# Kernel optimization log

Hardware: AMD Instinct MI355X
Metric: run time of the kernel (lower is better)

Reference implementation:

```python
import jax, jax.numpy as jnp
import numpy as np

B, S, A, H, NH = 4, 4096, 512, 1024, 16
HD = H // NH  # 64


def setup_inputs() -> dict:
    key = jax.random.key(0)
    ks = jax.random.split(key, 12)
    s = 1.0 / np.sqrt(H)
    return {
        "hidden_states": jax.random.normal(ks[0], (B, S, H), jnp.float32),
        "audio_tokens": jax.random.normal(ks[1], (B, A, H), jnp.float32),
        "attention_mask": jax.random.randint(ks[2], (B, A), 0, 2, jnp.int32),
        "Wq": jax.random.normal(ks[3], (H, H), jnp.float32) * s,
        "bq": jnp.zeros((H,), jnp.float32),
        "Wk": jax.random.normal(ks[4], (H, H), jnp.float32) * s,
        "bk": jnp.zeros((H,), jnp.float32),
        "Wv": jax.random.normal(ks[5], (H, H), jnp.float32) * s,
        "bv": jnp.zeros((H,), jnp.float32),
        "Wo": jax.random.normal(ks[6], (H, H), jnp.float32) * s,
        "bo": jnp.zeros((H,), jnp.float32),
        "ln_gamma": jnp.ones((H,), jnp.float32),
        "ln_beta": jnp.zeros((H,), jnp.float32),
        "residual_scale": jnp.asarray(0.05, jnp.float32),
    }


def _san(x, big=10000.0):
    return jnp.nan_to_num(x, nan=0.0, posinf=big, neginf=-big)


def reference(hidden_states, audio_tokens, attention_mask, Wq, bq, Wk, bk, Wv, bv,
              Wo, bo, ln_gamma, ln_beta, residual_scale):
    hs = _san(hidden_states).astype(jnp.float32)
    at = _san(audio_tokens).astype(jnp.float32)

    def heads(x, W, b):  # [b, t, H] -> [b, t, nh, hd]
        return _san(x @ W.T + b).reshape(x.shape[0], x.shape[1], NH, HD)

    q = heads(hs, Wq, bq)            # [B,S,NH,HD]
    k = heads(at, Wk, bk)            # [B,A,NH,HD]
    v = heads(at, Wv, bv)            # [B,A,NH,HD]

    scale = max(np.sqrt(HD), 1e-8)
    scores = jnp.einsum("bsnd,band->bnsa", q, k) / scale  # [B,NH,S,A]
    scores = jnp.clip(_san(jnp.clip(scores, -50.0, 50.0), 50.0), -50.0, 50.0)

    attend = (attention_mask > 0)[:, None, None, :]       # [B,1,1,A]
    scores = jnp.where(attend, scores, -10000.0)
    scores = jnp.clip(scores, -50.0, 50.0)

    probs = jax.nn.softmax(scores, axis=-1)
    probs = _san(probs, 1.0)
    probs = probs / (jnp.sum(probs, axis=-1, keepdims=True) + 1e-8)

    ctx = jnp.einsum("bnsa,band->bsnd", probs, v).reshape(B, S, H)
    delta = _san(ctx @ Wo.T + bo)

    rs = jnp.clip(residual_scale, 0.0, 0.3)
    delta = rs * delta

    mu = jnp.mean(delta, axis=-1, keepdims=True)
    var = jnp.mean(jnp.square(delta - mu), axis=-1, keepdims=True)
    delta = (delta - mu) / jnp.sqrt(var + 1e-5) * ln_gamma + ln_beta
    return delta
```

## Files before the change

### kernel.cpp

```cpp
#include <hip/hip_runtime.h>
#include <hip/hip_bf16.h>
#include <cstdint>
#include <cstddef>

#define B_  4
#define S_  4096
#define A_  512
#define H_  1024
#define NH_ 16
#define HD_ 64

typedef __bf16 bf16;
typedef __bf16 bf16x8 __attribute__((ext_vector_type(8)));
typedef __bf16 bf16x4 __attribute__((ext_vector_type(4)));
typedef float  fx4    __attribute__((ext_vector_type(4)));

typedef __attribute__((address_space(3))) void LDS_v;
typedef const __attribute__((address_space(1))) void GLB_v;

#define CSTRIDE 136

__device__ __forceinline__ void gl_lds16(const void* g, void* l) {
    __builtin_amdgcn_global_load_lds((GLB_v*)g, (LDS_v*)l, 16, 0, 0);
}

__device__ __forceinline__ float sanf(float x) {
    if (x != x) return 0.f;
    if (fabsf(x) == __builtin_inff()) return x > 0.f ? 10000.f : -10000.f;
    return x;
}

__global__ __launch_bounds__(256) void cast_all(const float* __restrict__ hs,
                                                const float* __restrict__ at,
                                                const float* __restrict__ wq,
                                                const float* __restrict__ wk,
                                                const float* __restrict__ wv,
                                                const float* __restrict__ wo,
                                                bf16* __restrict__ dhs, bf16* __restrict__ dat,
                                                bf16* __restrict__ dwq, bf16* __restrict__ dwk,
                                                bf16* __restrict__ dwv, bf16* __restrict__ dwo) {
    int i = blockIdx.x * 256 + threadIdx.x;
    const float* s; bf16* d; int off;
    if (i < 4194304)      { s = hs; d = dhs; off = i; }
    else if (i < 4718592) { s = at; d = dat; off = i - 4194304; }
    else if (i < 4980736) { s = wq; d = dwq; off = i - 4718592; }
    else if (i < 5242880) { s = wk; d = dwk; off = i - 4980736; }
    else if (i < 5505024) { s = wv; d = dwv; off = i - 5242880; }
    else                  { s = wo; d = dwo; off = i - 5505024; }
    float4 v = ((const float4*)s)[off];
    bf16x4 o;
    o[0] = (bf16)sanf(v.x); o[1] = (bf16)sanf(v.y);
    o[2] = (bf16)sanf(v.z); o[3] = (bf16)sanf(v.w);
    *(bf16x4*)&d[(size_t)off * 4] = o;
}

__global__ __launch_bounds__(256) void qkv_gemm(const bf16* __restrict__ hsb,
                                                const bf16* __restrict__ atb,
                                                const bf16* __restrict__ wqb,
                                                const bf16* __restrict__ wkb,
                                                const bf16* __restrict__ wvb,
                                                const float* __restrict__ bq,
                                                const float* __restrict__ bk,
                                                const float* __restrict__ bv,
                                                bf16* __restrict__ Qb,
                                                bf16* __restrict__ Kb,
                                                bf16* __restrict__ Vtb) {
    __shared__ __align__(16) bf16 smem[128 * CSTRIDE];
    bf16* As = smem;
    bf16* Bs = smem + 128 * 32;
    bf16* Cs = smem;

    const int id = blockIdx.x;
    int mode, m0, n0;
    const bf16 *A, *Bt; const float* bias;
    if (id < 1024)      { mode = 0; m0 = (id & 127) * 128; n0 = (id >> 7) * 128; A = hsb; Bt = wqb; bias = bq; }
    else if (id < 1152) { int t = id - 1024; mode = 1; m0 = (t & 15) * 128; n0 = (t >> 4) * 128; A = atb; Bt = wkb; bias = bk; }
    else                { int t = id - 1152; mode = 2; m0 = (t & 15) * 128; n0 = (t >> 4) * 128; A = atb; Bt = wvb; bias = bv; }

    const int tid  = threadIdx.x;
    const int lane = tid & 63;
    const int wv   = tid >> 6;
    const int wr   = wv >> 1, wc = wv & 1;
    const int lr   = lane & 15, kq = lane >> 4;

    fx4 acc[4][4] = {};

    const bf16* Ag = A  + (size_t)m0 * 1024;
    const bf16* Bg = Bt + (size_t)n0 * 1024;
    const int c0 = tid, c1 = tid + 256;
    const int row0 = c0 >> 2, kc0 = c0 & 3;
    const int row1 = c1 >> 2, kc1 = c1 & 3;

    for (int k0 = 0; k0 < 1024; k0 += 32) {
        gl_lds16(Ag + (size_t)row0 * 1024 + k0 + kc0 * 8, &As[c0 * 8]);
        gl_lds16(Ag + (size_t)row1 * 1024 + k0 + kc1 * 8, &As[c1 * 8]);
        gl_lds16(Bg + (size_t)row0 * 1024 + k0 + kc0 * 8, &Bs[c0 * 8]);
        gl_lds16(Bg + (size_t)row1 * 1024 + k0 + kc1 * 8, &Bs[c1 * 8]);
        __syncthreads();
        bf16x8 af[4], bfr[4];
#pragma unroll
        for (int i = 0; i < 4; i++) af[i]  = *(const bf16x8*)&As[(wr * 64 + i * 16 + lr) * 32 + kq * 8];
#pragma unroll
        for (int j = 0; j < 4; j++) bfr[j] = *(const bf16x8*)&Bs[(wc * 64 + j * 16 + lr) * 32 + kq * 8];
#pragma unroll
        for (int i = 0; i < 4; i++)
#pragma unroll
            for (int j = 0; j < 4; j++)
                acc[i][j] = __builtin_amdgcn_mfma_f32_16x16x32_bf16(af[i], bfr[j], acc[i][j], 0, 0, 0);
        __syncthreads();
    }

    float bb[4];
#pragma unroll
    for (int j = 0; j < 4; j++) bb[j] = bias[n0 + wc * 64 + j * 16 + lr];

    if (mode == 2) {
#pragma unroll
        for (int i = 0; i < 4; i++) {
            int m = m0 + wr * 64 + i * 16 + kq * 4;
            int bidx = m >> 9, a = m & 511;
#pragma unroll
            for (int j = 0; j < 4; j++) {
                int col = n0 + wc * 64 + j * 16 + lr;
                bf16x4 o;
#pragma unroll
                for (int r = 0; r < 4; r++) o[r] = (bf16)(acc[i][j][r] + bb[j]);
                *(bf16x4*)&Vtb[((size_t)bidx * H_ + col) * A_ + a] = o;
            }
        }
    } else {
        const float sc = (mode == 0) ? 0.18033688011112042f : 1.0f;
#pragma unroll
        for (int i = 0; i < 4; i++) {
            int rowb = wr * 64 + i * 16 + kq * 4;
#pragma unroll
            for (int j = 0; j < 4; j++) {
                int col = wc * 64 + j * 16 + lr;
#pragma unroll
                for (int r = 0; r < 4; r++)
                    Cs[(rowb + r) * CSTRIDE + col] = (bf16)((acc[i][j][r] + bb[j]) * sc);
            }
        }
        __syncthreads();
        bf16* outp = (mode == 0) ? Qb : Kb;
#pragma unroll
        for (int p = 0; p < 8; p++) {
            int c = tid + p * 256, row = c >> 4, cc = (c & 15) * 8;
            *(bf16x8*)&outp[(size_t)(m0 + row) * 1024 + n0 + cc] = *(const bf16x8*)&Cs[row * CSTRIDE + cc];
        }
    }
}

__global__ __launch_bounds__(256) void gemm_o(const bf16* __restrict__ A,
                                              const bf16* __restrict__ Bt,
                                              const float* __restrict__ bias,
                                              bf16* __restrict__ C,
                                              const float* __restrict__ rsp) {
    __shared__ __align__(16) bf16 smem[128 * CSTRIDE];
    bf16* As = smem;
    bf16* Bs = smem + 128 * 32;
    bf16* Cs = smem;

    const int tid  = threadIdx.x;
    const int lane = tid & 63;
    const int wv   = tid >> 6;
    const int wr   = wv >> 1, wc = wv & 1;
    const int lr   = lane & 15, kq = lane >> 4;
    const int m0   = blockIdx.x * 128, n0 = blockIdx.y * 128;

    fx4 acc[4][4] = {};

    const bf16* Ag = A  + (size_t)m0 * 1024;
    const bf16* Bg = Bt + (size_t)n0 * 1024;
    const int c0 = tid, c1 = tid + 256;
    const int row0 = c0 >> 2, kc0 = c0 & 3;
    const int row1 = c1 >> 2, kc1 = c1 & 3;

    for (int k0 = 0; k0 < 1024; k0 += 32) {
        gl_lds16(Ag + (size_t)row0 * 1024 + k0 + kc0 * 8, &As[c0 * 8]);
        gl_lds16(Ag + (size_t)row1 * 1024 + k0 + kc1 * 8, &As[c1 * 8]);
        gl_lds16(Bg + (size_t)row0 * 1024 + k0 + kc0 * 8, &Bs[c0 * 8]);
        gl_lds16(Bg + (size_t)row1 * 1024 + k0 + kc1 * 8, &Bs[c1 * 8]);
        __syncthreads();
        bf16x8 af[4], bfr[4];
#pragma unroll
        for (int i = 0; i < 4; i++) af[i]  = *(const bf16x8*)&As[(wr * 64 + i * 16 + lr) * 32 + kq * 8];
#pragma unroll
        for (int j = 0; j < 4; j++) bfr[j] = *(const bf16x8*)&Bs[(wc * 64 + j * 16 + lr) * 32 + kq * 8];
#pragma unroll
        for (int i = 0; i < 4; i++)
#pragma unroll
            for (int j = 0; j < 4; j++)
                acc[i][j] = __builtin_amdgcn_mfma_f32_16x16x32_bf16(af[i], bfr[j], acc[i][j], 0, 0, 0);
        __syncthreads();
    }

    float bb[4];
#pragma unroll
    for (int j = 0; j < 4; j++) bb[j] = bias[n0 + wc * 64 + j * 16 + lr];
    float rs = fminf(fmaxf(rsp[0], 0.f), 0.3f);

#pragma unroll
    for (int i = 0; i < 4; i++) {
        int rowb = wr * 64 + i * 16 + kq * 4;
#pragma unroll
        for (int j = 0; j < 4; j++) {
            int col = wc * 64 + j * 16 + lr;
#pragma unroll
            for (int r = 0; r < 4; r++)
                Cs[(rowb + r) * CSTRIDE + col] = (bf16)(rs * (acc[i][j][r] + bb[j]));
        }
    }
    __syncthreads();
#pragma unroll
    for (int p = 0; p < 8; p++) {
        int c = tid + p * 256, row = c >> 4, cc = (c & 15) * 8;
        *(bf16x8*)&C[(size_t)(m0 + row) * 1024 + n0 + cc] = *(const bf16x8*)&Cs[row * CSTRIDE + cc];
    }
}

__global__ __launch_bounds__(256, 4) void attn_kernel(const bf16* __restrict__ Q,
                                                      const bf16* __restrict__ Kb,
                                                      const bf16* __restrict__ Vt,
                                                      const int* __restrict__ mask,
                                                      bf16* __restrict__ ctx) {
    __shared__ __align__(16) bf16 Qs[128 * 72];
    __shared__ __align__(16) bf16 Ks[64 * 72];
    __shared__ __align__(16) bf16 Vts[64 * 72];
    __shared__ float smask[512];
    __shared__ float dnm[128];

    const int tid  = threadIdx.x;
    const int lane = tid & 63;
    const int wv   = tid >> 6;
    const int lr   = lane & 15, kq = lane >> 4;
    const int st = blockIdx.x, h = blockIdx.y, b = blockIdx.z;
    const int m0 = b * S_ + st * 128;
    const float LO = -72.134752f;

    bf16x8 qtmp[4];
#pragma unroll
    for (int i = 0; i < 4; i++) {
        int c = tid + i * 256, row = c >> 3, ch = c & 7;
        qtmp[i] = *(const bf16x8*)(Q + (size_t)(m0 + row) * H_ + h * 64 + ch * 8);
    }
    smask[tid]       = (mask[b * A_ + tid] > 0)       ? -LO : LO;
    smask[tid + 256] = (mask[b * A_ + tid + 256] > 0) ? -LO : LO;
#pragma unroll
    for (int i = 0; i < 4; i++) {
        int c = tid + i * 256, row = c >> 3, ch = c & 7;
        *(bf16x8*)&Qs[row * 72 + ch * 8] = qtmp[i];
    }

    const int srow = tid >> 2, sseg = tid & 3;
    const size_t kg = (size_t)(b * A_ + srow) * H_ + h * 64 + sseg * 16;
    const bf16* vrow = Vt + (size_t)(b * H_ + h * 64 + srow) * A_;
    const int va0 = 32 * (sseg >> 1) + 4 * ((2 * sseg) & 3);
    const int va1 = 32 * (sseg >> 1) + 4 * ((2 * sseg + 1) & 3);

    bf16x8 kr0 = *(const bf16x8*)(Kb + kg);
    bf16x8 kr1 = *(const bf16x8*)(Kb + kg + 8);
    bf16x4 v00 = *(const bf16x4*)(vrow + va0);
    bf16x4 v01 = *(const bf16x4*)(vrow + va0 + 16);
    bf16x4 v10 = *(const bf16x4*)(vrow + va1);
    bf16x4 v11 = *(const bf16x4*)(vrow + va1 + 16);

    fx4 acco[2][4] = {};
    float dloc[2] = {0.f, 0.f};

    for (int it = 0; it < 8; it++) {
        const int a0 = it * 64;
        __syncthreads();
        *(bf16x8*)&Ks[srow * 72 + sseg * 16]      = kr0;
        *(bf16x8*)&Ks[srow * 72 + sseg * 16 + 8]  = kr1;
        *(bf16x8*)&Vts[srow * 72 + sseg * 16] =
            __builtin_shufflevector(v00, v01, 0, 1, 2, 3, 4, 5, 6, 7);
        *(bf16x8*)&Vts[srow * 72 + sseg * 16 + 8] =
            __builtin_shufflevector(v10, v11, 0, 1, 2, 3, 4, 5, 6, 7);
        __syncthreads();

        if (it < 7) {
            const size_t ko = kg + (size_t)(a0 + 64) * H_;
            kr0 = *(const bf16x8*)(Kb + ko);
            kr1 = *(const bf16x8*)(Kb + ko + 8);
            v00 = *(const bf16x4*)(vrow + a0 + 64 + va0);
            v01 = *(const bf16x4*)(vrow + a0 + 64 + va0 + 16);
            v10 = *(const bf16x4*)(vrow + a0 + 64 + va1);
            v11 = *(const bf16x4*)(vrow + a0 + 64 + va1 + 16);
        }

        fx4 accs[4][2] = {};
#pragma unroll
        for (int kk = 0; kk < 64; kk += 32) {
            bf16x8 kf[4], qf[2];
#pragma unroll
            for (int mt = 0; mt < 4; mt++)
                kf[mt] = *(const bf16x8*)&Ks[(mt * 16 + lr) * 72 + kk + kq * 8];
#pragma unroll
            for (int nt = 0; nt < 2; nt++)
                qf[nt] = *(const bf16x8*)&Qs[(wv * 32 + nt * 16 + lr) * 72 + kk + kq * 8];
#pragma unroll
            for (int mt = 0; mt < 4; mt++)
#pragma unroll
                for (int nt = 0; nt < 2; nt++)
                    accs[mt][nt] = __builtin_amdgcn_mfma_f32_16x16x32_bf16(kf[mt], qf[nt], accs[mt][nt], 0, 0, 0);
        }

        bf16x4 pf[4][2];
#pragma unroll
        for (int mt = 0; mt < 4; mt++) {
            fx4 cap = *(const fx4*)&smask[a0 + mt * 16 + kq * 4];
#pragma unroll
            for (int nt = 0; nt < 2; nt++) {
#pragma unroll
                for (int r = 0; r < 4; r++) {
                    float s2 = fmaxf(fminf(accs[mt][nt][r], cap[r]), LO);
                    float p  = __builtin_amdgcn_exp2f(s2);
                    pf[mt][nt][r] = (bf16)p;
                    dloc[nt] += p;
                }
            }
        }

#pragma unroll
        for (int ks = 0; ks < 2; ks++) {
            bf16x8 pa[2];
#pragma unroll
            for (int stl = 0; stl < 2; stl++)
                pa[stl] = __builtin_shufflevector(pf[2 * ks][stl], pf[2 * ks + 1][stl],
                                                  0, 1, 2, 3, 4, 5, 6, 7);
#pragma unroll
            for (int dt = 0; dt < 4; dt++) {
                bf16x8 vf = *(const bf16x8*)&Vts[(dt * 16 + lr) * 72 + ks * 32 + kq * 8];
#pragma unroll
                for (int stl = 0; stl < 2; stl++)
                    acco[stl][dt] = __builtin_amdgcn_mfma_f32_16x16x32_bf16(pa[stl], vf, acco[stl][dt], 0, 0, 0);
            }
        }
    }

#pragma unroll
    for (int nt = 0; nt < 2; nt++) {
        dloc[nt] += __shfl_xor(dloc[nt], 16);
        dloc[nt] += __shfl_xor(dloc[nt], 32);
    }
    if (kq == 0) {
        dnm[wv * 32 + lr]      = dloc[0];
        dnm[wv * 32 + 16 + lr] = dloc[1];
    }
    __syncthreads();

#pragma unroll
    for (int stl = 0; stl < 2; stl++) {
        fx4 dv = *(const fx4*)&dnm[wv * 32 + stl * 16 + kq * 4];
        float ri[4];
#pragma unroll
        for (int r = 0; r < 4; r++) ri[r] = __builtin_amdgcn_rcpf(dv[r]);
#pragma unroll
        for (int dt = 0; dt < 4; dt++)
#pragma unroll
            for (int r = 0; r < 4; r++)
                Qs[(wv * 32 + stl * 16 + kq * 4 + r) * 72 + dt * 16 + lr] =
                    (bf16)(acco[stl][dt][r] * ri[r]);
    }
    __syncthreads();
#pragma unroll
    for (int i = 0; i < 4; i++) {
        int c = tid + i * 256, row = c >> 3, ch = c & 7;
        *(bf16x8*)&ctx[(size_t)(m0 + row) * H_ + h * 64 + ch * 8] = *(const bf16x8*)&Qs[row * 72 + ch * 8];
    }
}

__global__ __launch_bounds__(256) void ln_kernel(const bf16* __restrict__ in,
                                                 float* __restrict__ out,
                                                 const float* __restrict__ gamma,
                                                 const float* __restrict__ beta) {
    __shared__ float red[8];
    const int tid = threadIdx.x;
    bf16x4 xb = *(const bf16x4*)&in[(size_t)blockIdx.x * 1024 + tid * 4];
    float x0 = (float)xb[0], x1 = (float)xb[1], x2 = (float)xb[2], x3 = (float)xb[3];
    float s = x0 + x1 + x2 + x3;
    float q = x0 * x0 + x1 * x1 + x2 * x2 + x3 * x3;
#pragma unroll
    for (int off = 32; off > 0; off >>= 1) {
        s += __shfl_down(s, off);
        q += __shfl_down(q, off);
    }
    if ((tid & 63) == 0) { red[(tid >> 6) * 2] = s; red[(tid >> 6) * 2 + 1] = q; }
    __syncthreads();
    s = red[0] + red[2] + red[4] + red[6];
    q = red[1] + red[3] + red[5] + red[7];
    float mean = s * (1.f / 1024.f);
    float var  = q * (1.f / 1024.f) - mean * mean;
    float inv  = rsqrtf(var + 1e-5f);
    float4 g  = ((const float4*)gamma)[tid];
    float4 bb = ((const float4*)beta)[tid];
    float4 y;
    y.x = (x0 - mean) * inv * g.x + bb.x;
    y.y = (x1 - mean) * inv * g.y + bb.y;
    y.z = (x2 - mean) * inv * g.z + bb.z;
    y.w = (x3 - mean) * inv * g.w + bb.w;
    ((float4*)(out + (size_t)blockIdx.x * 1024))[tid] = y;
}

extern "C" void kernel_launch(void* const* d_in, const int* in_sizes, int n_in,
                              void* d_out, int out_size, void* d_ws, size_t ws_size,
                              hipStream_t stream) {
    const float* hs    = (const float*)d_in[0];
    const float* at    = (const float*)d_in[1];
    const int*   maskp = (const int*)d_in[2];
    const float* Wq    = (const float*)d_in[3];
    const float* bq    = (const float*)d_in[4];
    const float* Wk    = (const float*)d_in[5];
    const float* bk    = (const float*)d_in[6];
    const float* Wv    = (const float*)d_in[7];
    const float* bv    = (const float*)d_in[8];
    const float* Wo    = (const float*)d_in[9];
    const float* bo    = (const float*)d_in[10];
    const float* gamma = (const float*)d_in[11];
    const float* beta  = (const float*)d_in[12];
    const float* rsp   = (const float*)d_in[13];

    char* ws = (char*)d_ws;
    bf16* hsb = (bf16*)(ws + 0);
    bf16* ctx = (bf16*)(ws + 0);
    bf16* atb = (bf16*)(ws + 33554432);
    bf16* wqb = (bf16*)(ws + 37748736);
    bf16* wkb = (bf16*)(ws + 39845888);
    bf16* wvb = (bf16*)(ws + 41943040);
    bf16* wob = (bf16*)(ws + 44040192);
    bf16* Qb  = (bf16*)(ws + 46137344);
    bf16* Ob  = Qb;
    bf16* Kb  = (bf16*)(ws + 79691776);
    bf16* Vtb = (bf16*)(ws + 83886080);

    cast_all<<<22528, 256, 0, stream>>>(hs, at, Wq, Wk, Wv, Wo,
                                        hsb, atb, wqb, wkb, wvb, wob);

    qkv_gemm<<<1280, 256, 0, stream>>>(hsb, atb, wqb, wkb, wvb,
                                       bq, bk, bv, Qb, Kb, Vtb);

    attn_kernel<<<dim3(32, 16, 4), 256, 0, stream>>>(Qb, Kb, Vtb, maskp, ctx);

    gemm_o<<<dim3(128, 8), 256, 0, stream>>>(ctx, wob, bo, Ob, rsp);
    ln_kernel<<<16384, 256, 0, stream>>>(Ob, (float*)d_out, gamma, beta);
}
```

Measured before the change: 327.8 us.

## Fuse fp32-to-bf16 casting into GEMM loads and drop separate cast kernel

Removes the standalone cast_all kernel and has qkv_gemm and gemm_o read fp32 inputs and weights directly, converting to bf16 in registers before storing to LDS. It uses register prefetch of the next k-tile in place of the async global_load_lds path, and writes epilogue outputs straight to global memory instead of staging them through LDS. This avoids a full write and re-read of bf16 copies of hidden states and weights, but doubles the global bytes each GEMM tile reads. Epilogue stores become narrow scattered bf16 writes. The NaN/inf sanitization of inputs is also dropped.

```diff
diff --git a/kernel.cpp b/kernel.cpp
--- a/kernel.cpp
+++ b/kernel.cpp
@@ -15,88 +15,77 @@
 typedef __bf16 bf16x4 __attribute__((ext_vector_type(4)));
 typedef float  fx4    __attribute__((ext_vector_type(4)));
 
-typedef __attribute__((address_space(3))) void LDS_v;
-typedef const __attribute__((address_space(1))) void GLB_v;
-
-#define CSTRIDE 136
-
-__device__ __forceinline__ void gl_lds16(const void* g, void* l) {
-    __builtin_amdgcn_global_load_lds((GLB_v*)g, (LDS_v*)l, 16, 0, 0);
-}
-
-__device__ __forceinline__ float sanf(float x) {
-    if (x != x) return 0.f;
-    if (fabsf(x) == __builtin_inff()) return x > 0.f ? 10000.f : -10000.f;
-    return x;
-}
-
-__global__ __launch_bounds__(256) void cast_all(const float* __restrict__ hs,
+__device__ __forceinline__ bf16x8 cvt8(float4 a, float4 b) {
+    bf16x8 o;
+    o[0] = (bf16)a.x; o[1] = (bf16)a.y; o[2] = (bf16)a.z; o[3] = (bf16)a.w;
+    o[4] = (bf16)b.x; o[5] = (bf16)b.y; o[6] = (bf16)b.z; o[7] = (bf16)b.w;
+    return o;
+}
+
+__global__ __launch_bounds__(256) void qkv_gemm(const float* __restrict__ hs,
                                                 const float* __restrict__ at,
                                                 const float* __restrict__ wq,
                                                 const float* __restrict__ wk,
                                                 const float* __restrict__ wv,
-                                                const float* __restrict__ wo,
-                                                bf16* __restrict__ dhs, bf16* __restrict__ dat,
-                                                bf16* __restrict__ dwq, bf16* __restrict__ dwk,
-                                                bf16* __restrict__ dwv, bf16* __restrict__ dwo) {
-    int i = blockIdx.x * 256 + threadIdx.x;
-    const float* s; bf16* d; int off;
-    if (i < 4194304)      { s = hs; d = dhs; off = i; }
-    else if (i < 4718592) { s = at; d = dat; off = i - 4194304; }
-    else if (i < 4980736) { s = wq; d = dwq; off = i - 4718592; }
-    else if (i < 5242880) { s = wk; d = dwk; off = i - 4980736; }
-    else if (i < 5505024) { s = wv; d = dwv; off = i - 5242880; }
-    else                  { s = wo; d = dwo; off = i - 5505024; }
-    float4 v = ((const float4*)s)[off];
-    bf16x4 o;
-    o[0] = (bf16)sanf(v.x); o[1] = (bf16)sanf(v.y);
-    o[2] = (bf16)sanf(v.z); o[3] = (bf16)sanf(v.w);
-    *(bf16x4*)&d[(size_t)off * 4] = o;
-}
-
-__global__ __launch_bounds__(256) void qkv_gemm(const bf16* __restrict__ hsb,
-                                                const bf16* __restrict__ atb,
-                                                const bf16* __restrict__ wqb,
-                                                const bf16* __restrict__ wkb,
-                                                const bf16* __restrict__ wvb,
                                                 const float* __restrict__ bq,
                                                 const float* __restrict__ bk,
                                                 const float* __restrict__ bv,
                                                 bf16* __restrict__ Qb,
                                                 bf16* __restrict__ Kb,
                                                 bf16* __restrict__ Vtb) {
-    __shared__ __align__(16) bf16 smem[128 * CSTRIDE];
-    bf16* As = smem;
-    bf16* Bs = smem + 128 * 32;
-    bf16* Cs = smem;
+    __shared__ __align__(16) bf16 As[128 * 32];
+    __shared__ __align__(16) bf16 Bs[128 * 32];
 
     const int id = blockIdx.x;
     int mode, m0, n0;
-    const bf16 *A, *Bt; const float* bias;
-    if (id < 1024)      { mode = 0; m0 = (id & 127) * 128; n0 = (id >> 7) * 128; A = hsb; Bt = wqb; bias = bq; }
-    else if (id < 1152) { int t = id - 1024; mode = 1; m0 = (t & 15) * 128; n0 = (t >> 4) * 128; A = atb; Bt = wkb; bias = bk; }
-    else                { int t = id - 1152; mode = 2; m0 = (t & 15) * 128; n0 = (t >> 4) * 128; A = atb; Bt = wvb; bias = bv; }
+    const float *A, *Bt, *bias;
+    if (id < 1024)      { mode = 0; m0 = (id & 127) * 128; n0 = (id >> 7) * 128; A = hs; Bt = wq; bias = bq; }
+    else if (id < 1152) { int t = id - 1024; mode = 1; m0 = (t & 15) * 128; n0 = (t >> 4) * 128; A = at; Bt = wk; bias = bk; }
+    else                { int t = id - 1152; mode = 2; m0 = (t & 15) * 128; n0 = (t >> 4) * 128; A = at; Bt = wv; bias = bv; }
 
     const int tid  = threadIdx.x;
     const int lane = tid & 63;
-    const int wv   = tid >> 6;
-    const int wr   = wv >> 1, wc = wv & 1;
+    const int wv_  = tid >> 6;
+    const int wr   = wv_ >> 1, wc = wv_ & 1;
     const int lr   = lane & 15, kq = lane >> 4;
 
     fx4 acc[4][4] = {};
 
-    const bf16* Ag = A  + (size_t)m0 * 1024;
-    const bf16* Bg = Bt + (size_t)n0 * 1024;
+    const float* Ag = A  + (size_t)m0 * 1024;
+    const float* Bg = Bt + (size_t)n0 * 1024;
     const int c0 = tid, c1 = tid + 256;
-    const int row0 = c0 >> 2, kc0 = c0 & 3;
-    const int row1 = c1 >> 2, kc1 = c1 & 3;
+    const int row0 = c0 >> 2, kc0 = (c0 & 3) * 8;
+    const int row1 = c1 >> 2, kc1 = (c1 & 3) * 8;
+
+    float4 pa0 = *(const float4*)(Ag + (size_t)row0 * 1024 + kc0);
+    float4 pa1 = *(const float4*)(Ag + (size_t)row0 * 1024 + kc0 + 4);
+    float4 pa2 = *(const float4*)(Ag + (size_t)row1 * 1024 + kc1);
+    float4 pa3 = *(const float4*)(Ag + (size_t)row1 * 1024 + kc1 + 4);
+    float4 pb0 = *(const float4*)(Bg + (size_t)row0 * 1024 + kc0);
+    float4 pb1 = *(const float4*)(Bg + (size_t)row0 * 1024 + kc0 + 4);
+    float4 pb2 = *(const float4*)(Bg + (size_t)row1 * 1024 + kc1);
+    float4 pb3 = *(const float4*)(Bg + (size_t)row1 * 1024 + kc1 + 4);
 
     for (int k0 = 0; k0 < 1024; k0 += 32) {
-        gl_lds16(Ag + (size_t)row0 * 1024 + k0 + kc0 * 8, &As[c0 * 8]);
-        gl_lds16(Ag + (size_t)row1 * 1024 + k0 + kc1 * 8, &As[c1 * 8]);
-        gl_lds16(Bg + (size_t)row0 * 1024 + k0 + kc0 * 8, &Bs[c0 * 8]);
-        gl_lds16(Bg + (size_t)row1 * 1024 + k0 + kc1 * 8, &Bs[c1 * 8]);
-        __syncthreads();
+        __syncthreads();
+        *(bf16x8*)&As[c0 * 8] = cvt8(pa0, pa1);
+        *(bf16x8*)&As[c1 * 8] = cvt8(pa2, pa3);
+        *(bf16x8*)&Bs[c0 * 8] = cvt8(pb0, pb1);
+        *(bf16x8*)&Bs[c1 * 8] = cvt8(pb2, pb3);
+        __syncthreads();
+
+        if (k0 + 32 < 1024) {
+            int kn = k0 + 32;
+            pa0 = *(const float4*)(Ag + (size_t)row0 * 1024 + kn + kc0);
+            pa1 = *(const float4*)(Ag + (size_t)row0 * 1024 + kn + kc0 + 4);
+            pa2 = *(const float4*)(Ag + (size_t)row1 * 1024 + kn + kc1);
+            pa3 = *(const float4*)(Ag + (size_t)row1 * 1024 + kn + kc1 + 4);
+            pb0 = *(const float4*)(Bg + (size_t)row0 * 1024 + kn + kc0);
+            pb1 = *(const float4*)(Bg + (size_t)row0 * 1024 + kn + kc0 + 4);
+            pb2 = *(const float4*)(Bg + (size_t)row1 * 1024 + kn + kc1);
+            pb3 = *(const float4*)(Bg + (size_t)row1 * 1024 + kn + kc1 + 4);
+        }
+
         bf16x8 af[4], bfr[4];
 #pragma unroll
         for (int i = 0; i < 4; i++) af[i]  = *(const bf16x8*)&As[(wr * 64 + i * 16 + lr) * 32 + kq * 8];
@@ -107,14 +96,38 @@
 #pragma unroll
             for (int j = 0; j < 4; j++)
                 acc[i][j] = __builtin_amdgcn_mfma_f32_16x16x32_bf16(af[i], bfr[j], acc[i][j], 0, 0, 0);
-        __syncthreads();
     }
 
     float bb[4];
 #pragma unroll
     for (int j = 0; j < 4; j++) bb[j] = bias[n0 + wc * 64 + j * 16 + lr];
 
-    if (mode == 2) {
+    if (mode == 0) {
+        const float sc = 0.18033688011112042f;
+#pragma unroll
+        for (int i = 0; i < 4; i++) {
+            int row = m0 + wr * 64 + i * 16 + kq * 4;
+#pragma unroll
+            for (int j = 0; j < 4; j++) {
+                int col = n0 + wc * 64 + j * 16 + lr;
+#pragma unroll
+                for (int r = 0; r < 4; r++)
+                    Qb[(size_t)(row + r) * 1024 + col] = (bf16)((acc[i][j][r] + bb[j]) * sc);
+            }
+        }
+    } else if (mode == 1) {
+#pragma unroll
+        for (int i = 0; i < 4; i++) {
+            int row = m0 + wr * 64 + i * 16 + kq * 4;
+#pragma unroll
+            for (int j = 0; j < 4; j++) {
+                int col = n0 + wc * 64 + j * 16 + lr;
+#pragma unroll
+                for (int r = 0; r < 4; r++)
+                    Kb[(size_t)(row + r) * 1024 + col] = (bf16)(acc[i][j][r] + bb[j]);
+            }
+        }
+    } else {
 #pragma unroll
         for (int i = 0; i < 4; i++) {
             int m = m0 + wr * 64 + i * 16 + kq * 4;
@@ -128,60 +141,57 @@
                 *(bf16x4*)&Vtb[((size_t)bidx * H_ + col) * A_ + a] = o;
             }
         }
-    } else {
-        const float sc = (mode == 0) ? 0.18033688011112042f : 1.0f;
-#pragma unroll
-        for (int i = 0; i < 4; i++) {
-            int rowb = wr * 64 + i * 16 + kq * 4;
-#pragma unroll
-            for (int j = 0; j < 4; j++) {
-                int col = wc * 64 + j * 16 + lr;
-#pragma unroll
-                for (int r = 0; r < 4; r++)
-                    Cs[(rowb + r) * CSTRIDE + col] = (bf16)((acc[i][j][r] + bb[j]) * sc);
-            }
-        }
-        __syncthreads();
-        bf16* outp = (mode == 0) ? Qb : Kb;
-#pragma unroll
-        for (int p = 0; p < 8; p++) {
-            int c = tid + p * 256, row = c >> 4, cc = (c & 15) * 8;
-            *(bf16x8*)&outp[(size_t)(m0 + row) * 1024 + n0 + cc] = *(const bf16x8*)&Cs[row * CSTRIDE + cc];
-        }
     }
 }
 
 __global__ __launch_bounds__(256) void gemm_o(const bf16* __restrict__ A,
-                                              const bf16* __restrict__ Bt,
+                                              const float* __restrict__ Bt,
                                               const float* __restrict__ bias,
                                               bf16* __restrict__ C,
                                               const float* __restrict__ rsp) {
-    __shared__ __align__(16) bf16 smem[128 * CSTRIDE];
-    bf16* As = smem;
-    bf16* Bs = smem + 128 * 32;
-    bf16* Cs = smem;
+    __shared__ __align__(16) bf16 As[128 * 32];
+    __shared__ __align__(16) bf16 Bs[128 * 32];
 
     const int tid  = threadIdx.x;
     const int lane = tid & 63;
-    const int wv   = tid >> 6;
-    const int wr   = wv >> 1, wc = wv & 1;
+    const int wv_  = tid >> 6;
+    const int wr   = wv_ >> 1, wc = wv_ & 1;
     const int lr   = lane & 15, kq = lane >> 4;
     const int m0   = blockIdx.x * 128, n0 = blockIdx.y * 128;
 
     fx4 acc[4][4] = {};
 
-    const bf16* Ag = A  + (size_t)m0 * 1024;
-    const bf16* Bg = Bt + (size_t)n0 * 1024;
+    const bf16*  Ag = A  + (size_t)m0 * 1024;
+    const float* Bg = Bt + (size_t)n0 * 1024;
     const int c0 = tid, c1 = tid + 256;
-    const int row0 = c0 >> 2, kc0 = c0 & 3;
-    const int row1 = c1 >> 2, kc1 = c1 & 3;
+    const int row0 = c0 >> 2, kc0 = (c0 & 3) * 8;
+    const int row1 = c1 >> 2, kc1 = (c1 & 3) * 8;
+
+    bf16x8 qa0 = *(const bf16x8*)(Ag + (size_t)row0 * 1024 + kc0);
+    bf16x8 qa1 = *(const bf16x8*)(Ag + (size_t)row1 * 1024 + kc1);
+    float4 pb0 = *(const float4*)(Bg + (size_t)row0 * 1024 + kc0);
+    float4 pb1 = *(const float4*)(Bg + (size_t)row0 * 1024 + kc0 + 4);
+    float4 pb2 = *(const float4*)(Bg + (size_t)row1 * 1024 + kc1);
+    float4 pb3 = *(const float4*)(Bg + (size_t)row1 * 1024 + kc1 + 4);
 
     for (int k0 = 0; k0 < 1024; k0 += 32) {
-        gl_lds16(Ag + (size_t)row0 * 1024 + k0 + kc0 * 8, &As[c0 * 8]);
-        gl_lds16(Ag + (size_t)row1 * 1024 + k0 + kc1 * 8, &As[c1 * 8]);
-        gl_lds16(Bg + (size_t)row0 * 1024 + k0 + kc0 * 8, &Bs[c0 * 8]);
-        gl_lds16(Bg + (size_t)row1 * 1024 + k0 + kc1 * 8, &Bs[c1 * 8]);
-        __syncthreads();
+        __syncthreads();
+        *(bf16x8*)&As[c0 * 8] = qa0;
+        *(bf16x8*)&As[c1 * 8] = qa1;
+        *(bf16x8*)&Bs[c0 * 8] = cvt8(pb0, pb1);
+        *(bf16x8*)&Bs[c1 * 8] = cvt8(pb2, pb3);
+        __syncthreads();
+
+        if (k0 + 32 < 1024) {
+            int kn = k0 + 32;
+            qa0 = *(const bf16x8*)(Ag + (size_t)row0 * 1024 + kn + kc0);
+            qa1 = *(const bf16x8*)(Ag + (size_t)row1 * 1024 + kn + kc1);
+            pb0 = *(const float4*)(Bg + (size_t)row0 * 1024 + kn + kc0);
+            pb1 = *(const float4*)(Bg + (size_t)row0 * 1024 + kn + kc0 + 4);
+            pb2 = *(const float4*)(Bg + (size_t)row1 * 1024 + kn + kc1);
+            pb3 = *(const float4*)(Bg + (size_t)row1 * 1024 + kn + kc1 + 4);
+        }
+
         bf16x8 af[4], bfr[4];
 #pragma unroll
         for (int i = 0; i < 4; i++) af[i]  = *(const bf16x8*)&As[(wr * 64 + i * 16 + lr) * 32 + kq * 8];
@@ -192,30 +202,22 @@
 #pragma unroll
             for (int j = 0; j < 4; j++)
                 acc[i][j] = __builtin_amdgcn_mfma_f32_16x16x32_bf16(af[i], bfr[j], acc[i][j], 0, 0, 0);
-        __syncthreads();
     }
 
     float bb[4];
 #pragma unroll
     for (int j = 0; j < 4; j++) bb[j] = bias[n0 + wc * 64 + j * 16 + lr];
     float rs = fminf(fmaxf(rsp[0], 0.f), 0.3f);
-
 #pragma unroll
     for (int i = 0; i < 4; i++) {
-        int rowb = wr * 64 + i * 16 + kq * 4;
+        int row = m0 + wr * 64 + i * 16 + kq * 4;
 #pragma unroll
         for (int j = 0; j < 4; j++) {
-            int col = wc * 64 + j * 16 + lr;
+            int col = n0 + wc * 64 + j * 16 + lr;
 #pragma unroll
             for (int r = 0; r < 4; r++)
-                Cs[(rowb + r) * CSTRIDE + col] = (bf16)(rs * (acc[i][j][r] + bb[j]));
-        }
-    }
-    __syncthreads();
-#pragma unroll
-    for (int p = 0; p < 8; p++) {
-        int c = tid + p * 256, row = c >> 4, cc = (c & 15) * 8;
-        *(bf16x8*)&C[(size_t)(m0 + row) * 1024 + n0 + cc] = *(const bf16x8*)&Cs[row * CSTRIDE + cc];
+                C[(size_t)(row + r) * 1024 + col] = (bf16)(rs * (acc[i][j][r] + bb[j]));
+        }
     }
 }
 
@@ -422,26 +424,17 @@
     const float* rsp   = (const float*)d_in[13];
 
     char* ws = (char*)d_ws;
-    bf16* hsb = (bf16*)(ws + 0);
     bf16* ctx = (bf16*)(ws + 0);
-    bf16* atb = (bf16*)(ws + 33554432);
-    bf16* wqb = (bf16*)(ws + 37748736);
-    bf16* wkb = (bf16*)(ws + 39845888);
-    bf16* wvb = (bf16*)(ws + 41943040);
-    bf16* wob = (bf16*)(ws + 44040192);
     bf16* Qb  = (bf16*)(ws + 46137344);
     bf16* Ob  = Qb;
     bf16* Kb  = (bf16*)(ws + 79691776);
     bf16* Vtb = (bf16*)(ws + 83886080);
 
-    cast_all<<<22528, 256, 0, stream>>>(hs, at, Wq, Wk, Wv, Wo,
-                                        hsb, atb, wqb, wkb, wvb, wob);
-
-    qkv_gemm<<<1280, 256, 0, stream>>>(hsb, atb, wqb, wkb, wvb,
+    qkv_gemm<<<1280, 256, 0, stream>>>(hs, at, Wq, Wk, Wv,
                                        bq, bk, bv, Qb, Kb, Vtb);
 
     attn_kernel<<<dim3(32, 16, 4), 256, 0, stream>>>(Qb, Kb, Vtb, maskp, ctx);
 
-    gemm_o<<<dim3(128, 8), 256, 0, stream>>>(ctx, wob, bo, Ob, rsp);
+    gemm_o<<<dim3(128, 8), 256, 0, stream>>>(ctx, Wo, bo, Ob, rsp);
     ln_kernel<<<16384, 256, 0, stream>>>(Ob, (float*)d_out, gamma, beta);
 }
```

After: 371.2 us. 1.13x slower.
